# Performance work log

Hardware: AMD Instinct MI355X
Metric: run time of the kernel (lower is better)

## Reference

```python
import jax, jax.numpy as jnp
import numpy as np

B, T, D, H = 4, 1024, 1024, 16
HD = D // H
MAX_LEN = 1024


def _layernorm(x, g, b, eps=1e-5):
    mu = jnp.mean(x, axis=-1, keepdims=True)
    var = jnp.var(x, axis=-1, keepdims=True)
    return (x - mu) * jax.lax.rsqrt(var + eps) * g + b


def setup_inputs() -> dict:
    key = jax.random.key(0)
    ks = jax.random.split(key, 12)
    s = 1.0 / np.sqrt(D)
    return {
        "src": jax.random.normal(ks[0], (B, T, D), jnp.float32),
        "Wqkv": jax.random.uniform(ks[1], (D, 3 * D), jnp.float32, -s, s),
        "bqkv": jnp.zeros((3 * D,), jnp.float32),
        "Wo": jax.random.uniform(ks[2], (D, D), jnp.float32, -s, s),
        "bo": jnp.zeros((D,), jnp.float32),
        "rel_bias": 0.02 * jax.random.normal(ks[3], (H, 2 * MAX_LEN - 1), jnp.float32),
        "temperature": jnp.float32(1.0),
        "W1": jax.random.uniform(ks[4], (D, 4 * D), jnp.float32, -s, s),
        "b1": jnp.zeros((4 * D,), jnp.float32),
        "W2": jax.random.uniform(ks[5], (4 * D, D), jnp.float32, -1.0 / np.sqrt(4 * D), 1.0 / np.sqrt(4 * D)),
        "b2": jnp.zeros((D,), jnp.float32),
        "ff_scale": jnp.ones((1,), jnp.float32),
        "gamma1": jnp.ones((D,), jnp.float32),
        "beta1": jnp.zeros((D,), jnp.float32),
        "gamma2": jnp.ones((D,), jnp.float32),
        "beta2": jnp.zeros((D,), jnp.float32),
    }


def reference(src, Wqkv, bqkv, Wo, bo, rel_bias, temperature, W1, b1, W2, b2,
              ff_scale, gamma1, beta1, gamma2, beta2):
    b, t, c = src.shape
    # QKV projection -> [3, B, H, T, HD]
    qkv = (src @ Wqkv + bqkv).reshape(b, t, 3, H, HD).transpose(2, 0, 3, 1, 4)
    q, k, v = qkv[0], qkv[1], qkv[2]
    temp = jnp.maximum(temperature, 0.01)  # clamp(min=0.01)
    logits = jnp.einsum("bhqd,bhkd->bhqk", q, k) / temp
    # relative position bias gather: [H, T, T]
    pos = jnp.arange(t)
    rel = pos[None, :] - pos[:, None] + (t - 1)
    logits = logits + rel_bias[:, rel][None]
    attn_weights = jax.nn.softmax(logits, axis=-1)
    attn_out = jnp.einsum("bhqk,bhkd->bhqd", attn_weights, v)
    attn_out = attn_out.transpose(0, 2, 1, 3).reshape(b, t, c) @ Wo + bo
    x = _layernorm(src + attn_out, gamma1, beta1)
    ff = jax.nn.gelu(x @ W1 + b1, approximate=False) @ W2 + b2
    out = _layernorm(x + ff_scale * ff, gamma2, beta2)
    return (out, attn_weights)
```

## Files before the change

### kernel.cpp

```cpp
#include <hip/hip_runtime.h>
#include <math.h>

#define BB 4
#define TT 1024
#define DM 1024
#define NH 16
#define HD 64
#define DFF 4096
#define N3 3072

typedef unsigned short u16;
typedef __attribute__((ext_vector_type(4))) float f32x4;
typedef __attribute__((ext_vector_type(8))) short s16x8;

__device__ __forceinline__ u16 f2bf(float f) {
    union { float f; unsigned u; } v; v.f = f;
    unsigned u = v.u;
    u += 0x7fffu + ((u >> 16) & 1u);
    return (u16)(u >> 16);
}
__device__ __forceinline__ float bf2f(u16 h) {
    union { unsigned u; float f; } v; v.u = ((unsigned)h) << 16;
    return v.f;
}

__device__ __forceinline__ void async_copy16(const void* g, void* l) {
    __builtin_amdgcn_global_load_lds(
        (const __attribute__((address_space(1))) unsigned int*)g,
        (__attribute__((address_space(3))) unsigned int*)l, 16, 0, 0);
}

__global__ __launch_bounds__(256) void cvt_kernel(const float* __restrict__ in,
                                                  u16* __restrict__ out, int n) {
    int i = (blockIdx.x * 256 + threadIdx.x) * 4;
    if (i + 3 < n) {
        out[i + 0] = f2bf(in[i + 0]);
        out[i + 1] = f2bf(in[i + 1]);
        out[i + 2] = f2bf(in[i + 2]);
        out[i + 3] = f2bf(in[i + 3]);
    }
}

template<int TIN>
__global__ __launch_bounds__(256) void transpose_kernel(const void* __restrict__ inv,
                                                        u16* __restrict__ out, int R, int C) {
    __shared__ float tile[32][33];
    const float* inF = (const float*)inv;
    const u16* inH = (const u16*)inv;
    size_t boff = (size_t)blockIdx.z * R * C;
    int c0 = blockIdx.x * 32, r0 = blockIdx.y * 32;
    int tx = threadIdx.x & 31, ty = threadIdx.x >> 5;
    for (int i = 0; i < 4; i++) {
        int r = r0 + ty + i * 8, c = c0 + tx;
        float v = (TIN == 0) ? inF[boff + (size_t)r * C + c] : bf2f(inH[boff + (size_t)r * C + c]);
        tile[ty + i * 8][tx] = v;
    }
    __syncthreads();
    for (int i = 0; i < 4; i++) {
        int rr = r0 + tx, cc = c0 + ty + i * 8;
        out[boff + (size_t)cc * R + rr] = f2bf(tile[tx][ty + i * 8]);
    }
}

template<int EPI>
__global__ __launch_bounds__(256) void gemm_kernel(const u16* __restrict__ A,
                                                   const u16* __restrict__ BT,
                                                   const float* __restrict__ bias,
                                                   u16* __restrict__ out0, u16* __restrict__ out1,
                                                   u16* __restrict__ out2, int M, int N, int K) {
    __shared__ u16 As[128 * 32];
    __shared__ u16 Bs[128 * 32];
    const int tid = threadIdx.x;
    const int lane = tid & 63;
    const int wave = tid >> 6;
    const int quad = lane >> 4;
    const int l15 = lane & 15;
    const int wy = wave >> 1, wx = wave & 1;
    const int m0 = blockIdx.y * 128;
    const int n0 = blockIdx.x * 128;

    const int ai0 = wave * 2, ai1 = wave * 2 + 1;
    const u16* aG0 = A + (size_t)(m0 + ai0 * 16 + (lane >> 2)) * K + (lane & 3) * 8;
    const u16* aG1 = A + (size_t)(m0 + ai1 * 16 + (lane >> 2)) * K + (lane & 3) * 8;
    const u16* bG0 = BT + (size_t)(n0 + ai0 * 16 + (lane >> 2)) * K + (lane & 3) * 8;
    const u16* bG1 = BT + (size_t)(n0 + ai1 * 16 + (lane >> 2)) * K + (lane & 3) * 8;
    u16* aL0 = &As[ai0 * 512];
    u16* aL1 = &As[ai1 * 512];
    u16* bL0 = &Bs[ai0 * 512];
    u16* bL1 = &Bs[ai1 * 512];

    f32x4 acc[4][4] = {};

    for (int k0 = 0; k0 < K; k0 += 32) {
        async_copy16(aG0 + k0, aL0);
        async_copy16(aG1 + k0, aL1);
        async_copy16(bG0 + k0, bL0);
        async_copy16(bG1 + k0, bL1);
        __syncthreads();
        s16x8 af[4], bf[4];
#pragma unroll
        for (int i = 0; i < 4; i++)
            af[i] = *(const s16x8*)&As[(wy * 64 + i * 16 + l15) * 32 + quad * 8];
#pragma unroll
        for (int j = 0; j < 4; j++)
            bf[j] = *(const s16x8*)&Bs[(wx * 64 + j * 16 + l15) * 32 + quad * 8];
#pragma unroll
        for (int i = 0; i < 4; i++)
#pragma unroll
            for (int j = 0; j < 4; j++)
                acc[i][j] = __builtin_amdgcn_mfma_f32_16x16x32_bf16(af[i], bf[j], acc[i][j], 0, 0, 0);
        __syncthreads();
    }

#pragma unroll
    for (int i = 0; i < 4; i++) {
#pragma unroll
        for (int j = 0; j < 4; j++) {
            f32x4 c = acc[i][j];
            int gn = n0 + wx * 64 + j * 16 + l15;
            float bv = bias[gn];
#pragma unroll
            for (int r = 0; r < 4; r++) {
                int gm = m0 + wy * 64 + i * 16 + quad * 4 + r;
                float v = c[r] + bv;
                if (EPI == 2) v = 0.5f * v * (1.f + erff(v * 0.70710678118f));
                if (EPI == 0 || EPI == 2) {
                    out0[(size_t)gm * N + gn] = f2bf(v);
                } else {
                    int which = gn >> 10, h = (gn >> 6) & 15, d = gn & 63;
                    int bb = gm >> 10, t = gm & 1023;
                    u16* dst = (which == 0) ? out0 : ((which == 1) ? out1 : out2);
                    dst[((size_t)(bb * NH + h) * TT + t) * HD + d] = f2bf(v);
                }
            }
        }
    }
}

__global__ __launch_bounds__(256) void attn_kernel(const u16* __restrict__ Qb,
                                                   const u16* __restrict__ Kb,
                                                   const u16* __restrict__ VTb,
                                                   const float* __restrict__ rel_bias,
                                                   const float* __restrict__ temp_p,
                                                   float* __restrict__ probs_out,
                                                   u16* __restrict__ attn_out) {
    __shared__ u16 Qs[16 * 72];
    __shared__ u16 Ps[16 * 1032];
    __shared__ float red[2][4][16];
    __shared__ float Op[4][16][64];

    const int tid = threadIdx.x;
    const int lane = tid & 63, wave = tid >> 6, quad = lane >> 4, l15 = lane & 15;
    const int q0 = blockIdx.x * 16;
    const int h = blockIdx.y, b = blockIdx.z;
    const int bh = b * NH + h;
    const size_t headoff = (size_t)bh * TT * HD;

    float temp = fmaxf(temp_p[0], 0.01f);
    const float itemp = 1.f / temp;

    {
        int row = tid >> 4, col = (tid & 15) * 4;
        const u16* srcp = Qb + headoff + (size_t)(q0 + row) * HD + col;
        *(uint2*)&Qs[row * 72 + col] = *(const uint2*)srcp;
    }
    __syncthreads();

    s16x8 a0 = *(const s16x8*)&Qs[l15 * 72 + quad * 8];
    s16x8 a1 = *(const s16x8*)&Qs[l15 * 72 + 32 + quad * 8];
    f32x4 s[16];
    const u16* Kh = Kb + headoff;
#pragma unroll
    for (int nt = 0; nt < 16; nt++) {
        int key = wave * 256 + nt * 16 + l15;
        const u16* kp = Kh + (size_t)key * HD;
        s16x8 b0 = *(const s16x8*)(kp + quad * 8);
        s16x8 b1 = *(const s16x8*)(kp + 32 + quad * 8);
        f32x4 acc = {};
        acc = __builtin_amdgcn_mfma_f32_16x16x32_bf16(a0, b0, acc, 0, 0, 0);
        acc = __builtin_amdgcn_mfma_f32_16x16x32_bf16(a1, b1, acc, 0, 0, 0);
#pragma unroll
        for (int r = 0; r < 4; r++) {
            int q = q0 + quad * 4 + r;
            acc[r] = acc[r] * itemp + rel_bias[h * 2047 + (key - q + 1023)];
        }
        s[nt] = acc;
    }

    float lm[4];
#pragma unroll
    for (int r = 0; r < 4; r++) {
        float m = s[0][r];
#pragma unroll
        for (int nt = 1; nt < 16; nt++) m = fmaxf(m, s[nt][r]);
        for (int off = 8; off >= 1; off >>= 1) m = fmaxf(m, __shfl_xor(m, off));
        lm[r] = m;
    }
    if (l15 == 0)
        for (int r = 0; r < 4; r++) red[0][wave][quad * 4 + r] = lm[r];
    __syncthreads();
    float rm[4];
#pragma unroll
    for (int r = 0; r < 4; r++) {
        int row = quad * 4 + r;
        rm[r] = fmaxf(fmaxf(red[0][0][row], red[0][1][row]),
                      fmaxf(red[0][2][row], red[0][3][row]));
    }

    float ls[4] = {0.f, 0.f, 0.f, 0.f};
#pragma unroll
    for (int nt = 0; nt < 16; nt++)
#pragma unroll
        for (int r = 0; r < 4; r++) {
            float p = __expf(s[nt][r] - rm[r]);
            s[nt][r] = p;
            ls[r] += p;
        }
#pragma unroll
    for (int r = 0; r < 4; r++) {
        float v = ls[r];
        for (int off = 8; off >= 1; off >>= 1) v += __shfl_xor(v, off);
        ls[r] = v;
    }
    if (l15 == 0)
        for (int r = 0; r < 4; r++) red[1][wave][quad * 4 + r] = ls[r];
    __syncthreads();
    float inv[4];
#pragma unroll
    for (int r = 0; r < 4; r++) {
        int row = quad * 4 + r;
        inv[r] = 1.f / (red[1][0][row] + red[1][1][row] + red[1][2][row] + red[1][3][row]);
    }

    float* prow = probs_out + ((size_t)bh * TT + q0) * TT;
#pragma unroll
    for (int nt = 0; nt < 16; nt++) {
        int key = wave * 256 + nt * 16 + l15;
#pragma unroll
        for (int r = 0; r < 4; r++) {
            int row = quad * 4 + r;
            prow[(size_t)row * TT + key] = s[nt][r] * inv[r];
            Ps[row * 1032 + key] = f2bf(s[nt][r]);
        }
    }
    __syncthreads();

    f32x4 o[4] = {};
    const u16* Vh = VTb + headoff;
#pragma unroll
    for (int ks = 0; ks < 8; ks++) {
        int k0 = wave * 256 + ks * 32;
        s16x8 pa = *(const s16x8*)&Ps[l15 * 1032 + k0 + quad * 8];
#pragma unroll
        for (int nt = 0; nt < 4; nt++) {
            int d = nt * 16 + l15;
            s16x8 vb = *(const s16x8*)(Vh + (size_t)d * TT + k0 + quad * 8);
            o[nt] = __builtin_amdgcn_mfma_f32_16x16x32_bf16(pa, vb, o[nt], 0, 0, 0);
        }
    }
#pragma unroll
    for (int nt = 0; nt < 4; nt++)
#pragma unroll
        for (int r = 0; r < 4; r++) Op[wave][quad * 4 + r][nt * 16 + l15] = o[nt][r];
    __syncthreads();

    {
        int m = tid >> 4, dc = (tid & 15) * 4;
        float acc4[4];
#pragma unroll
        for (int c = 0; c < 4; c++)
            acc4[c] = Op[0][m][dc + c] + Op[1][m][dc + c] + Op[2][m][dc + c] + Op[3][m][dc + c];
        float rinv = 1.f / (red[1][0][m] + red[1][1][m] + red[1][2][m] + red[1][3][m]);
        u16 pk[4];
#pragma unroll
        for (int c = 0; c < 4; c++) pk[c] = f2bf(acc4[c] * rinv);
        *(uint2*)&attn_out[((size_t)(b * TT + q0 + m)) * DM + h * HD + dc] = *(uint2*)pk;
    }
}

template<int MODE>
__global__ __launch_bounds__(256) void ln_kernel(const float* __restrict__ af32,
                                                 const u16* __restrict__ abf,
                                                 const u16* __restrict__ addbf,
                                                 const float* __restrict__ scale_p,
                                                 const float* __restrict__ gamma,
                                                 const float* __restrict__ beta,
                                                 float* __restrict__ outf,
                                                 u16* __restrict__ outbf) {
    __shared__ float red[2][4];
    int row = blockIdx.x;
    int tid = threadIdx.x;
    float scale = (MODE == 1) ? scale_p[0] : 1.f;
    int c0 = tid * 4;
    size_t base = (size_t)row * DM + c0;
    float x[4];
#pragma unroll
    for (int c = 0; c < 4; c++) {
        float v = (MODE == 0) ? af32[base + c] : bf2f(abf[base + c]);
        v += scale * bf2f(addbf[base + c]);
        x[c] = v;
    }
    float s = x[0] + x[1] + x[2] + x[3];
    float sq = x[0] * x[0] + x[1] * x[1] + x[2] * x[2] + x[3] * x[3];
    for (int off = 32; off >= 1; off >>= 1) {
        s += __shfl_xor(s, off);
        sq += __shfl_xor(sq, off);
    }
    int wave = tid >> 6;
    if ((tid & 63) == 0) {
        red[0][wave] = s;
        red[1][wave] = sq;
    }
    __syncthreads();
    s = red[0][0] + red[0][1] + red[0][2] + red[0][3];
    sq = red[1][0] + red[1][1] + red[1][2] + red[1][3];
    float mu = s * (1.f / DM);
    float var = sq * (1.f / DM) - mu * mu;
    float rs = rsqrtf(var + 1e-5f);
#pragma unroll
    for (int c = 0; c < 4; c++) {
        float y = (x[c] - mu) * rs * gamma[c0 + c] + beta[c0 + c];
        if (MODE == 0) outbf[base + c] = f2bf(y);
        else outf[base + c] = y;
    }
}

#define OFF_SRCBF 0UL
#define OFF_WQKVT 8388608UL
#define OFF_WOT 14680064UL
#define OFF_W1T 16777216UL
#define OFF_W2T 25165824UL
#define OFF_Q 33554432UL
#define OFF_K 41943040UL
#define OFF_V 50331648UL
#define OFF_VT 58720256UL
#define OFF_ATTNO 67108864UL
#define OFF_PROJ 75497472UL
#define OFF_XBF 83886080UL
#define OFF_H1 92274688UL

extern "C" void kernel_launch(void* const* d_in, const int* in_sizes, int n_in,
                              void* d_out, int out_size, void* d_ws, size_t ws_size,
                              hipStream_t stream) {
    const float* src = (const float*)d_in[0];
    const float* Wqkv = (const float*)d_in[1];
    const float* bqkv = (const float*)d_in[2];
    const float* Wo = (const float*)d_in[3];
    const float* bo = (const float*)d_in[4];
    const float* relb = (const float*)d_in[5];
    const float* temp = (const float*)d_in[6];
    const float* W1 = (const float*)d_in[7];
    const float* b1 = (const float*)d_in[8];
    const float* W2 = (const float*)d_in[9];
    const float* b2 = (const float*)d_in[10];
    const float* ffs = (const float*)d_in[11];
    const float* g1 = (const float*)d_in[12];
    const float* be1 = (const float*)d_in[13];
    const float* g2 = (const float*)d_in[14];
    const float* be2 = (const float*)d_in[15];

    char* ws = (char*)d_ws;
    u16* srcbf = (u16*)(ws + OFF_SRCBF);
    u16* WqkvT = (u16*)(ws + OFF_WQKVT);
    u16* WoT = (u16*)(ws + OFF_WOT);
    u16* W1T = (u16*)(ws + OFF_W1T);
    u16* W2T = (u16*)(ws + OFF_W2T);
    u16* Qb = (u16*)(ws + OFF_Q);
    u16* Kb = (u16*)(ws + OFF_K);
    u16* Vb = (u16*)(ws + OFF_V);
    u16* VTb = (u16*)(ws + OFF_VT);
    u16* attnbf = (u16*)(ws + OFF_ATTNO);
    u16* projbf = (u16*)(ws + OFF_PROJ);
    u16* xbf = (u16*)(ws + OFF_XBF);
    u16* h1bf = (u16*)(ws + OFF_H1);

    float* out_f = (float*)d_out;
    float* probs = out_f + (size_t)BB * TT * DM;

    cvt_kernel<<<4096, 256, 0, stream>>>(src, srcbf, BB * TT * DM);
    transpose_kernel<0><<<dim3(N3 / 32, DM / 32, 1), 256, 0, stream>>>(Wqkv, WqkvT, DM, N3);
    transpose_kernel<0><<<dim3(DM / 32, DM / 32, 1), 256, 0, stream>>>(Wo, WoT, DM, DM);
    transpose_kernel<0><<<dim3(DFF / 32, DM / 32, 1), 256, 0, stream>>>(W1, W1T, DM, DFF);
    transpose_kernel<0><<<dim3(DM / 32, DFF / 32, 1), 256, 0, stream>>>(W2, W2T, DFF, DM);
    gemm_kernel<1><<<dim3(N3 / 128, (BB * TT) / 128), 256, 0, stream>>>(
        srcbf, WqkvT, bqkv, Qb, Kb, Vb, BB * TT, N3, DM);
    transpose_kernel<1><<<dim3(HD / 32, TT / 32, BB * NH), 256, 0, stream>>>(Vb, VTb, TT, HD);
    attn_kernel<<<dim3(TT / 16, NH, BB), 256, 0, stream>>>(Qb, Kb, VTb, relb, temp, probs, attnbf);
    gemm_kernel<0><<<dim3(DM / 128, (BB * TT) / 128), 256, 0, stream>>>(
        attnbf, WoT, bo, projbf, nullptr, nullptr, BB * TT, DM, DM);
    ln_kernel<0><<<BB * TT, 256, 0, stream>>>(src, nullptr, projbf, nullptr, g1, be1, nullptr, xbf);
    gemm_kernel<2><<<dim3(DFF / 128, (BB * TT) / 128), 256, 0, stream>>>(
        xbf, W1T, b1, h1bf, nullptr, nullptr, BB * TT, DFF, DM);
    gemm_kernel<0><<<dim3(DM / 128, (BB * TT) / 128), 256, 0, stream>>>(
        h1bf, W2T, b2, projbf, nullptr, nullptr, BB * TT, DM, DFF);
    ln_kernel<1><<<BB * TT, 256, 0, stream>>>(nullptr, xbf, projbf, ffs, g2, be2, out_f, nullptr);
}
```

Baseline: 760.2 us.

## Split-K the N=1024 GEMMs into fp32 partials and widen attention to 8 waves

The Wo and W2 projection GEMMs, which launch only 256 blocks, are split along K into 2 and 4 slices. Each slice writes fp32 partial sums, and the layernorm kernels add the partials and the bias. This raises block count to fill more compute units, at the cost of extra fp32 partial traffic. The attention kernel moves from 4 to 8 waves per 16-query block, stages the relative-bias window in shared memory, and normalizes probabilities before the PV product. It also reuses the P buffer for the cross-wave output reduction.

```diff
diff --git a/kernel.cpp b/kernel.cpp
--- a/kernel.cpp
+++ b/kernel.cpp
@@ -66,8 +66,9 @@
 __global__ __launch_bounds__(256) void gemm_kernel(const u16* __restrict__ A,
                                                    const u16* __restrict__ BT,
                                                    const float* __restrict__ bias,
-                                                   u16* __restrict__ out0, u16* __restrict__ out1,
-                                                   u16* __restrict__ out2, int M, int N, int K) {
+                                                   void* __restrict__ out0v,
+                                                   u16* __restrict__ out1, u16* __restrict__ out2,
+                                                   int M, int N, int Kstride, int Ksl) {
     __shared__ u16 As[128 * 32];
     __shared__ u16 Bs[128 * 32];
     const int tid = threadIdx.x;
@@ -78,12 +79,13 @@
     const int wy = wave >> 1, wx = wave & 1;
     const int m0 = blockIdx.y * 128;
     const int n0 = blockIdx.x * 128;
+    const int koff = blockIdx.z * Ksl;
 
     const int ai0 = wave * 2, ai1 = wave * 2 + 1;
-    const u16* aG0 = A + (size_t)(m0 + ai0 * 16 + (lane >> 2)) * K + (lane & 3) * 8;
-    const u16* aG1 = A + (size_t)(m0 + ai1 * 16 + (lane >> 2)) * K + (lane & 3) * 8;
-    const u16* bG0 = BT + (size_t)(n0 + ai0 * 16 + (lane >> 2)) * K + (lane & 3) * 8;
-    const u16* bG1 = BT + (size_t)(n0 + ai1 * 16 + (lane >> 2)) * K + (lane & 3) * 8;
+    const u16* aG0 = A + (size_t)(m0 + ai0 * 16 + (lane >> 2)) * Kstride + (lane & 3) * 8;
+    const u16* aG1 = A + (size_t)(m0 + ai1 * 16 + (lane >> 2)) * Kstride + (lane & 3) * 8;
+    const u16* bG0 = BT + (size_t)(n0 + ai0 * 16 + (lane >> 2)) * Kstride + (lane & 3) * 8;
+    const u16* bG1 = BT + (size_t)(n0 + ai1 * 16 + (lane >> 2)) * Kstride + (lane & 3) * 8;
     u16* aL0 = &As[ai0 * 512];
     u16* aL1 = &As[ai1 * 512];
     u16* bL0 = &Bs[ai0 * 512];
@@ -91,7 +93,7 @@
 
     f32x4 acc[4][4] = {};
 
-    for (int k0 = 0; k0 < K; k0 += 32) {
+    for (int k0 = koff; k0 < koff + Ksl; k0 += 32) {
         async_copy16(aG0 + k0, aL0);
         async_copy16(aG1 + k0, aL1);
         async_copy16(bG0 + k0, bL0);
@@ -112,24 +114,27 @@
         __syncthreads();
     }
 
+    const size_t MN = (size_t)M * N;
 #pragma unroll
     for (int i = 0; i < 4; i++) {
 #pragma unroll
         for (int j = 0; j < 4; j++) {
             f32x4 c = acc[i][j];
             int gn = n0 + wx * 64 + j * 16 + l15;
-            float bv = bias[gn];
+            float bv = (EPI == 3) ? 0.f : bias[gn];
 #pragma unroll
             for (int r = 0; r < 4; r++) {
                 int gm = m0 + wy * 64 + i * 16 + quad * 4 + r;
                 float v = c[r] + bv;
                 if (EPI == 2) v = 0.5f * v * (1.f + erff(v * 0.70710678118f));
                 if (EPI == 0 || EPI == 2) {
-                    out0[(size_t)gm * N + gn] = f2bf(v);
+                    ((u16*)out0v)[(size_t)gm * N + gn] = f2bf(v);
+                } else if (EPI == 3) {
+                    ((float*)out0v)[(size_t)blockIdx.z * MN + (size_t)gm * N + gn] = v;
                 } else {
                     int which = gn >> 10, h = (gn >> 6) & 15, d = gn & 63;
                     int bb = gm >> 10, t = gm & 1023;
-                    u16* dst = (which == 0) ? out0 : ((which == 1) ? out1 : out2);
+                    u16* dst = (which == 0) ? (u16*)out0v : ((which == 1) ? out1 : out2);
                     dst[((size_t)(bb * NH + h) * TT + t) * HD + d] = f2bf(v);
                 }
             }
@@ -137,17 +142,17 @@
     }
 }
 
-__global__ __launch_bounds__(256) void attn_kernel(const u16* __restrict__ Qb,
+__global__ __launch_bounds__(512) void attn_kernel(const u16* __restrict__ Qb,
                                                    const u16* __restrict__ Kb,
                                                    const u16* __restrict__ VTb,
                                                    const float* __restrict__ rel_bias,
                                                    const float* __restrict__ temp_p,
                                                    float* __restrict__ probs_out,
                                                    u16* __restrict__ attn_out) {
-    __shared__ u16 Qs[16 * 72];
-    __shared__ u16 Ps[16 * 1032];
-    __shared__ float red[2][4][16];
-    __shared__ float Op[4][16][64];
+    __shared__ __align__(16) u16 Qs[16 * 72];
+    __shared__ __align__(16) u16 Ps[16 * 1032];
+    __shared__ float red[2][8][16];
+    __shared__ float RB[1040];
 
     const int tid = threadIdx.x;
     const int lane = tid & 63, wave = tid >> 6, quad = lane >> 4, l15 = lane & 15;
@@ -159,7 +164,9 @@
     float temp = fmaxf(temp_p[0], 0.01f);
     const float itemp = 1.f / temp;
 
-    {
+    for (int i = tid; i < 1039; i += 512)
+        RB[i] = rel_bias[h * 2047 + (1008 - q0) + i];
+    if (tid < 256) {
         int row = tid >> 4, col = (tid & 15) * 4;
         const u16* srcp = Qb + headoff + (size_t)(q0 + row) * HD + col;
         *(uint2*)&Qs[row * 72 + col] = *(const uint2*)srcp;
@@ -168,11 +175,11 @@
 
     s16x8 a0 = *(const s16x8*)&Qs[l15 * 72 + quad * 8];
     s16x8 a1 = *(const s16x8*)&Qs[l15 * 72 + 32 + quad * 8];
-    f32x4 s[16];
+    f32x4 s[8];
     const u16* Kh = Kb + headoff;
 #pragma unroll
-    for (int nt = 0; nt < 16; nt++) {
-        int key = wave * 256 + nt * 16 + l15;
+    for (int nt = 0; nt < 8; nt++) {
+        int key = wave * 128 + nt * 16 + l15;
         const u16* kp = Kh + (size_t)key * HD;
         s16x8 b0 = *(const s16x8*)(kp + quad * 8);
         s16x8 b1 = *(const s16x8*)(kp + 32 + quad * 8);
@@ -180,10 +187,8 @@
         acc = __builtin_amdgcn_mfma_f32_16x16x32_bf16(a0, b0, acc, 0, 0, 0);
         acc = __builtin_amdgcn_mfma_f32_16x16x32_bf16(a1, b1, acc, 0, 0, 0);
 #pragma unroll
-        for (int r = 0; r < 4; r++) {
-            int q = q0 + quad * 4 + r;
-            acc[r] = acc[r] * itemp + rel_bias[h * 2047 + (key - q + 1023)];
-        }
+        for (int r = 0; r < 4; r++)
+            acc[r] = acc[r] * itemp + RB[key - (quad * 4 + r) + 15];
         s[nt] = acc;
     }
 
@@ -192,7 +197,7 @@
     for (int r = 0; r < 4; r++) {
         float m = s[0][r];
 #pragma unroll
-        for (int nt = 1; nt < 16; nt++) m = fmaxf(m, s[nt][r]);
+        for (int nt = 1; nt < 8; nt++) m = fmaxf(m, s[nt][r]);
         for (int off = 8; off >= 1; off >>= 1) m = fmaxf(m, __shfl_xor(m, off));
         lm[r] = m;
     }
@@ -203,13 +208,15 @@
 #pragma unroll
     for (int r = 0; r < 4; r++) {
         int row = quad * 4 + r;
-        rm[r] = fmaxf(fmaxf(red[0][0][row], red[0][1][row]),
-                      fmaxf(red[0][2][row], red[0][3][row]));
+        float m = red[0][0][row];
+#pragma unroll
+        for (int w = 1; w < 8; w++) m = fmaxf(m, red[0][w][row]);
+        rm[r] = m;
     }
 
     float ls[4] = {0.f, 0.f, 0.f, 0.f};
 #pragma unroll
-    for (int nt = 0; nt < 16; nt++)
+    for (int nt = 0; nt < 8; nt++)
 #pragma unroll
         for (int r = 0; r < 4; r++) {
             float p = __expf(s[nt][r] - rm[r]);
@@ -229,18 +236,22 @@
 #pragma unroll
     for (int r = 0; r < 4; r++) {
         int row = quad * 4 + r;
-        inv[r] = 1.f / (red[1][0][row] + red[1][1][row] + red[1][2][row] + red[1][3][row]);
+        float v = red[1][0][row];
+#pragma unroll
+        for (int w = 1; w < 8; w++) v += red[1][w][row];
+        inv[r] = 1.f / v;
     }
 
     float* prow = probs_out + ((size_t)bh * TT + q0) * TT;
 #pragma unroll
-    for (int nt = 0; nt < 16; nt++) {
-        int key = wave * 256 + nt * 16 + l15;
+    for (int nt = 0; nt < 8; nt++) {
+        int key = wave * 128 + nt * 16 + l15;
 #pragma unroll
         for (int r = 0; r < 4; r++) {
             int row = quad * 4 + r;
-            prow[(size_t)row * TT + key] = s[nt][r] * inv[r];
-            Ps[row * 1032 + key] = f2bf(s[nt][r]);
+            float pn = s[nt][r] * inv[r];
+            prow[(size_t)row * TT + key] = pn;
+            Ps[row * 1032 + key] = f2bf(pn);
         }
     }
     __syncthreads();
@@ -248,8 +259,8 @@
     f32x4 o[4] = {};
     const u16* Vh = VTb + headoff;
 #pragma unroll
-    for (int ks = 0; ks < 8; ks++) {
-        int k0 = wave * 256 + ks * 32;
+    for (int ks = 0; ks < 4; ks++) {
+        int k0 = wave * 128 + ks * 32;
         s16x8 pa = *(const s16x8*)&Ps[l15 * 1032 + k0 + quad * 8];
 #pragma unroll
         for (int nt = 0; nt < 4; nt++) {
@@ -258,47 +269,57 @@
             o[nt] = __builtin_amdgcn_mfma_f32_16x16x32_bf16(pa, vb, o[nt], 0, 0, 0);
         }
     }
+    __syncthreads();
+    float* OpF = (float*)Ps;
 #pragma unroll
     for (int nt = 0; nt < 4; nt++)
 #pragma unroll
-        for (int r = 0; r < 4; r++) Op[wave][quad * 4 + r][nt * 16 + l15] = o[nt][r];
+        for (int r = 0; r < 4; r++)
+            OpF[(wave * 16 + quad * 4 + r) * 64 + nt * 16 + l15] = o[nt][r];
     __syncthreads();
 
     {
-        int m = tid >> 4, dc = (tid & 15) * 4;
-        float acc4[4];
-#pragma unroll
-        for (int c = 0; c < 4; c++)
-            acc4[c] = Op[0][m][dc + c] + Op[1][m][dc + c] + Op[2][m][dc + c] + Op[3][m][dc + c];
-        float rinv = 1.f / (red[1][0][m] + red[1][1][m] + red[1][2][m] + red[1][3][m]);
-        u16 pk[4];
-#pragma unroll
-        for (int c = 0; c < 4; c++) pk[c] = f2bf(acc4[c] * rinv);
-        *(uint2*)&attn_out[((size_t)(b * TT + q0 + m)) * DM + h * HD + dc] = *(uint2*)pk;
-    }
-}
-
-template<int MODE>
+        int m = tid >> 5, dc = (tid & 31) * 2;
+        float a0v = 0.f, a1v = 0.f;
+#pragma unroll
+        for (int w = 0; w < 8; w++) {
+            a0v += OpF[(w * 16 + m) * 64 + dc];
+            a1v += OpF[(w * 16 + m) * 64 + dc + 1];
+        }
+        u16 pk[2] = {f2bf(a0v), f2bf(a1v)};
+        *(unsigned*)&attn_out[((size_t)(b * TT + q0 + m)) * DM + h * HD + dc] = *(unsigned*)pk;
+    }
+}
+
+template<int MODE, int KS>
 __global__ __launch_bounds__(256) void ln_kernel(const float* __restrict__ af32,
                                                  const u16* __restrict__ abf,
-                                                 const u16* __restrict__ addbf,
+                                                 const float* __restrict__ part,
+                                                 const float* __restrict__ biasN,
                                                  const float* __restrict__ scale_p,
                                                  const float* __restrict__ gamma,
                                                  const float* __restrict__ beta,
                                                  float* __restrict__ outf,
                                                  u16* __restrict__ outbf) {
     __shared__ float red[2][4];
+    const size_t MN = (size_t)BB * TT * DM;
     int row = blockIdx.x;
     int tid = threadIdx.x;
-    float scale = (MODE == 1) ? scale_p[0] : 1.f;
+    float sc = (MODE == 1) ? scale_p[0] : 1.f;
     int c0 = tid * 4;
     size_t base = (size_t)row * DM + c0;
+    float4 a = *(const float4*)(biasN + c0);
+    float acc[4] = {a.x, a.y, a.z, a.w};
+#pragma unroll
+    for (int kz = 0; kz < KS; kz++) {
+        float4 p = *(const float4*)(part + kz * MN + base);
+        acc[0] += p.x; acc[1] += p.y; acc[2] += p.z; acc[3] += p.w;
+    }
     float x[4];
 #pragma unroll
     for (int c = 0; c < 4; c++) {
-        float v = (MODE == 0) ? af32[base + c] : bf2f(abf[base + c]);
-        v += scale * bf2f(addbf[base + c]);
-        x[c] = v;
+        float b0 = (MODE == 0) ? af32[base + c] : bf2f(abf[base + c]);
+        x[c] = b0 + sc * acc[c];
     }
     float s = x[0] + x[1] + x[2] + x[3];
     float sq = x[0] * x[0] + x[1] * x[1] + x[2] * x[2] + x[3] * x[3];
@@ -335,9 +356,9 @@
 #define OFF_V 50331648UL
 #define OFF_VT 58720256UL
 #define OFF_ATTNO 67108864UL
-#define OFF_PROJ 75497472UL
 #define OFF_XBF 83886080UL
 #define OFF_H1 92274688UL
+#define OFF_PART 134217728UL
 
 extern "C" void kernel_launch(void* const* d_in, const int* in_sizes, int n_in,
                               void* d_out, int out_size, void* d_ws, size_t ws_size,
@@ -370,9 +391,9 @@
     u16* Vb = (u16*)(ws + OFF_V);
     u16* VTb = (u16*)(ws + OFF_VT);
     u16* attnbf = (u16*)(ws + OFF_ATTNO);
-    u16* projbf = (u16*)(ws + OFF_PROJ);
     u16* xbf = (u16*)(ws + OFF_XBF);
     u16* h1bf = (u16*)(ws + OFF_H1);
+    float* partF = (float*)(ws + OFF_PART);
 
     float* out_f = (float*)d_out;
     float* probs = out_f + (size_t)BB * TT * DM;
@@ -382,16 +403,18 @@
     transpose_kernel<0><<<dim3(DM / 32, DM / 32, 1), 256, 0, stream>>>(Wo, WoT, DM, DM);
     transpose_kernel<0><<<dim3(DFF / 32, DM / 32, 1), 256, 0, stream>>>(W1, W1T, DM, DFF);
     transpose_kernel<0><<<dim3(DM / 32, DFF / 32, 1), 256, 0, stream>>>(W2, W2T, DFF, DM);
-    gemm_kernel<1><<<dim3(N3 / 128, (BB * TT) / 128), 256, 0, stream>>>(
-        srcbf, WqkvT, bqkv, Qb, Kb, Vb, BB * TT, N3, DM);
+    gemm_kernel<1><<<dim3(N3 / 128, (BB * TT) / 128, 1), 256, 0, stream>>>(
+        srcbf, WqkvT, bqkv, Qb, Kb, Vb, BB * TT, N3, DM, DM);
     transpose_kernel<1><<<dim3(HD / 32, TT / 32, BB * NH), 256, 0, stream>>>(Vb, VTb, TT, HD);
-    attn_kernel<<<dim3(TT / 16, NH, BB), 256, 0, stream>>>(Qb, Kb, VTb, relb, temp, probs, attnbf);
-    gemm_kernel<0><<<dim3(DM / 128, (BB * TT) / 128), 256, 0, stream>>>(
-        attnbf, WoT, bo, projbf, nullptr, nullptr, BB * TT, DM, DM);
-    ln_kernel<0><<<BB * TT, 256, 0, stream>>>(src, nullptr, projbf, nullptr, g1, be1, nullptr, xbf);
-    gemm_kernel<2><<<dim3(DFF / 128, (BB * TT) / 128), 256, 0, stream>>>(
-        xbf, W1T, b1, h1bf, nullptr, nullptr, BB * TT, DFF, DM);
-    gemm_kernel<0><<<dim3(DM / 128, (BB * TT) / 128), 256, 0, stream>>>(
-        h1bf, W2T, b2, projbf, nullptr, nullptr, BB * TT, DM, DFF);
-    ln_kernel<1><<<BB * TT, 256, 0, stream>>>(nullptr, xbf, projbf, ffs, g2, be2, out_f, nullptr);
-}
+    attn_kernel<<<dim3(TT / 16, NH, BB), 512, 0, stream>>>(Qb, Kb, VTb, relb, temp, probs, attnbf);
+    gemm_kernel<3><<<dim3(DM / 128, (BB * TT) / 128, 2), 256, 0, stream>>>(
+        attnbf, WoT, nullptr, partF, nullptr, nullptr, BB * TT, DM, DM, DM / 2);
+    ln_kernel<0, 2><<<BB * TT, 256, 0, stream>>>(src, nullptr, partF, bo, nullptr, g1, be1,
+                                                 nullptr, xbf);
+    gemm_kernel<2><<<dim3(DFF / 128, (BB * TT) / 128, 1), 256, 0, stream>>>(
+        xbf, W1T, b1, h1bf, nullptr, nullptr, BB * TT, DFF, DM, DM);
+    gemm_kernel<3><<<dim3(DM / 128, (BB * TT) / 128, 4), 256, 0, stream>>>(
+        h1bf, W2T, nullptr, partF, nullptr, nullptr, BB * TT, DM, DFF, DFF / 4);
+    ln_kernel<1, 4><<<BB * TT, 256, 0, stream>>>(nullptr, xbf, partF, b2, ffs, g2, be2,
+                                                 out_f, nullptr);
+}
```

Result: faster. 704.1 us (-7.4%).
